# Kernel optimization log

Hardware: AMD Instinct MI355X
Metric: run time of the kernel (lower is better)

The kernel has to match this reference:

```python
import jax, jax.numpy as jnp
import numpy as np

N_NODES = 50000
N_EDGES = 1600000
IN_DIM = 512
HID = 128  # conv1 out = 2*HID = 256, conv2 out = HID = 128
EPS = 1e-5


def gcn_conv(x, src, dst, W, b, n_nodes):
    """PyG GCNConv: x' = D^{-1/2} (A + I) D^{-1/2} (x W) + b (self loops added)."""
    h = x @ W  # [N, out]
    loop = jnp.arange(n_nodes, dtype=src.dtype)
    s = jnp.concatenate([src, loop])  # sources incl. self loops
    d = jnp.concatenate([dst, loop])  # targets incl. self loops
    ones = jnp.ones(s.shape[0], dtype=h.dtype)
    deg = jax.ops.segment_sum(ones, d, num_segments=n_nodes)  # in-degree on targets
    dis = jnp.where(deg > 0, jax.lax.rsqrt(jnp.maximum(deg, 1.0)), 0.0)
    norm = dis[s] * dis[d]  # [E+N]
    msg = norm[:, None] * h[s]  # gather + scale, [E+N, out]
    out = jax.ops.segment_sum(msg, d, num_segments=n_nodes)  # scatter-add
    return out + b


def batch_norm(x, gamma, beta):
    """BatchNorm1d with batch statistics (biased variance), eps=1e-5."""
    mean = jnp.mean(x, axis=0)
    var = jnp.mean(jnp.square(x - mean), axis=0)
    return (x - mean) * jax.lax.rsqrt(var + EPS) * gamma + beta


def setup_inputs() -> dict:
    key = jax.random.key(0)
    ks = jax.random.split(key, 8)
    x = jax.random.normal(ks[0], (N_NODES, IN_DIM), dtype=jnp.float32)
    edge_index = jax.random.randint(ks[1], (2, N_EDGES), 0, N_NODES, dtype=jnp.int64)
    d1 = 2 * HID
    W1 = jax.random.normal(ks[2], (IN_DIM, d1), dtype=jnp.float32) / np.sqrt(IN_DIM)
    b1 = jnp.zeros((d1,), dtype=jnp.float32)
    gamma1 = jnp.ones((d1,), dtype=jnp.float32)
    beta1 = jnp.zeros((d1,), dtype=jnp.float32)
    W2 = jax.random.normal(ks[3], (d1, HID), dtype=jnp.float32) / np.sqrt(d1)
    b2 = jnp.zeros((HID,), dtype=jnp.float32)
    gamma2 = jnp.ones((HID,), dtype=jnp.float32)
    beta2 = jnp.zeros((HID,), dtype=jnp.float32)
    return {"x": x, "edge_index": edge_index, "W1": W1, "b1": b1,
            "gamma1": gamma1, "beta1": beta1, "W2": W2, "b2": b2,
            "gamma2": gamma2, "beta2": beta2}


def reference(x, edge_index, W1, b1, gamma1, beta1, W2, b2, gamma2, beta2):
    src, dst = edge_index[0], edge_index[1]
    h = gcn_conv(x, src, dst, W1, b1, N_NODES)
    h = batch_norm(h, gamma1, beta1)
    h = jax.nn.relu(h)
    # dropout: identity in eval mode (deterministic reference)
    h = gcn_conv(h, src, dst, W2, b2, N_NODES)
    h = batch_norm(h, gamma2, beta2)
    return h
```

## Files before the change

kernel.cpp:

```cpp
#include <hip/hip_runtime.h>
#include <hip/hip_bf16.h>


#define NN 50000
#define NE 1600000
#define DIN 512
#define D1 256
#define D2 128
#define EPSV 1e-5f
#define NBUCK 16
#define BSZ 3125
#define NDB 128
#define NPB 391
#define CAP 16384

typedef __attribute__((ext_vector_type(8))) short bf16x8_t;
typedef __attribute__((ext_vector_type(4))) float f32x4_t;

__device__ __forceinline__ float bf2f(unsigned short u) {
  return __uint_as_float(((unsigned int)u) << 16);
}
__device__ __forceinline__ unsigned short f2bf(float f) {
  unsigned int u = __float_as_uint(f);
  u += 0x7fffu + ((u >> 16) & 1u);
  return (unsigned short)(u >> 16);
}
__device__ __forceinline__ unsigned int pk2(float a, float b) {
  __hip_bfloat162 h = __float22bfloat162_rn(make_float2(a, b));
  union { __hip_bfloat162 h; unsigned int u; } c;
  c.h = h;
  return c.u;
}

__global__ __launch_bounds__(256) void k_part_prep(const int* __restrict__ src,
                                                   const int* __restrict__ dst,
                                                   int* __restrict__ gcursor,
                                                   unsigned int* __restrict__ part,
                                                   const float* __restrict__ W1,
                                                   const float* __restrict__ W2,
                                                   unsigned short* __restrict__ W1t,
                                                   unsigned short* __restrict__ W2t) {
  __shared__ int hist[NDB];
  __shared__ int curs[NDB];
  const int t = threadIdx.x;
  if (blockIdx.x < 256) {
    const int EB = NE / 256;
    const int e0 = blockIdx.x * EB;
    if (t < NDB) hist[t] = 0;
    __syncthreads();
    for (int i = t; i < EB; i += 256) {
      int d = dst[e0 + i];
      atomicAdd(&hist[d / NPB], 1);
    }
    __syncthreads();
    if (t < NDB) {
      int c = hist[t];
      curs[t] = (c > 0) ? atomicAdd(&gcursor[t], c) : 0;
    }
    __syncthreads();
    for (int i = t; i < EB; i += 256) {
      int s = src[e0 + i];
      int d = dst[e0 + i];
      int b = d / NPB;
      int dl = d - b * NPB;
      int sb = (unsigned)s / BSZ;
      unsigned int w = (unsigned)s | ((unsigned)dl << 16) | ((unsigned)sb << 25);
      int pos = atomicAdd(&curs[b], 1);
      if (pos < CAP) part[(size_t)b * CAP + pos] = w;
    }
  } else {
    int i = (blockIdx.x - 256) * 256 + t;
    if (i < DIN * D1) {
      int n = i / DIN, k = i - n * DIN;
      W1t[i] = f2bf(W1[(size_t)k * D1 + n]);
    } else {
      int j = i - DIN * D1;
      int n = j / D1, k = j - n * D1;
      W2t[j] = f2bf(W2[(size_t)k * D2 + n]);
    }
  }
}

__global__ void k_bscan(const int* __restrict__ gcursor, int* __restrict__ ebase) {
  __shared__ int s[NDB];
  int t = threadIdx.x;
  int v = gcursor[t];
  s[t] = v;
  __syncthreads();
  for (int off = 1; off < NDB; off <<= 1) {
    int a = (t >= off) ? s[t - off] : 0;
    __syncthreads();
    s[t] += a;
    __syncthreads();
  }
  ebase[t] = s[t] - v;
  if (t == NDB - 1) ebase[NDB] = s[t];
}

__global__ __launch_bounds__(256) void k_build_gemm1(const unsigned int* __restrict__ part,
                                                     const int* __restrict__ gcursor,
                                                     const int* __restrict__ ebase,
                                                     int* __restrict__ row_ptr,
                                                     float* __restrict__ dis,
                                                     int* __restrict__ col,
                                                     const float* __restrict__ A,
                                                     const unsigned short* __restrict__ Bt,
                                                     unsigned short* __restrict__ C, int M) {
  __shared__ __align__(16) char smem[40960];
  const int t = threadIdx.x;
  if (blockIdx.x < NDB) {
    const int NC = NPB * NBUCK;
    int* cnt = (int*)smem;
    int* tsum = (int*)(smem + 25024);
    const int b = blockIdx.x;
    int m = gcursor[b];
    if (m > CAP) m = CAP;
    const int base = ebase[b];
    const unsigned int* my = part + (size_t)b * CAP;
    for (int i = t; i < NC; i += 256) cnt[i] = 0;
    __syncthreads();
    for (int i = t; i < m; i += 256) {
      unsigned int w = my[i];
      atomicAdd(&cnt[((w >> 16) & 0x1ff) * NBUCK + (w >> 25)], 1);
    }
    __syncthreads();
    const int CHK = (NC + 255) / 256;
    int i0 = t * CHK;
    int sum = 0;
    for (int i = 0; i < CHK; i++) {
      int idx = i0 + i;
      if (idx < NC) sum += cnt[idx];
    }
    tsum[t] = sum;
    __syncthreads();
    for (int off = 1; off < 256; off <<= 1) {
      int a = (t >= off) ? tsum[t - off] : 0;
      __syncthreads();
      tsum[t] += a;
      __syncthreads();
    }
    int run = tsum[t] - sum;
    for (int i = 0; i < CHK; i++) {
      int idx = i0 + i;
      if (idx < NC) {
        int c = cnt[idx];
        cnt[idx] = run;
        run += c;
      }
    }
    __syncthreads();
    const int n0 = b * NPB;
    for (int dl = t; dl < NPB; dl += 256) {
      int n = n0 + dl;
      if (n < NN) {
        int st = cnt[dl * NBUCK];
        int en = (dl * NBUCK + NBUCK < NC) ? cnt[dl * NBUCK + NBUCK] : m;
        row_ptr[n] = base + st;
        dis[n] = rsqrtf((float)(en - st + 1));
      }
    }
    if (b == NDB - 1 && t == 0) row_ptr[NN] = base + m;
    __syncthreads();
    for (int i = t; i < m; i += 256) {
      unsigned int w = my[i];
      int pos = atomicAdd(&cnt[((w >> 16) & 0x1ff) * NBUCK + (w >> 25)], 1);
      col[base + pos] = w & 0xffff;
    }
  } else {
    unsigned short* As = (unsigned short*)smem;
    unsigned short* Bs = (unsigned short*)(smem + 8192);
    const int wave = t >> 6, lane = t & 63;
    const int m0 = (blockIdx.x - NDB) * 64;
    const int wn = wave * 64;
    const int l8 = lane >> 3;
    const int lbs = (lane & 7) ^ l8;
    const int row_c = lane & 15, quad = lane >> 4;

    f32x4_t acc[4][4];
#pragma unroll
    for (int i = 0; i < 4; i++)
#pragma unroll
      for (int j = 0; j < 4; j++) acc[i][j] = (f32x4_t){0.f, 0.f, 0.f, 0.f};

    for (int k0 = 0; k0 < DIN; k0 += 64) {
#pragma unroll
      for (int j = 0; j < 8; j++) {
        int chunk = wave * 8 + j;
        int row = chunk * 8 + l8;
        const unsigned short* g = Bt + (size_t)row * DIN + k0 + lbs * 8;
        __builtin_amdgcn_global_load_lds(
            (const __attribute__((address_space(1))) unsigned int*)g,
            (__attribute__((address_space(3))) unsigned int*)(Bs + chunk * 512), 16, 0, 0);
      }
#pragma unroll
      for (int i = 0; i < 2; i++) {
        int bid = i * 256 + t;
        int row = bid >> 3, pb = bid & 7;
        int lb = pb ^ (row & 7);
        int gm = m0 + row;
        if (gm >= M) gm = M - 1;
        const float4* s = (const float4*)(A + (size_t)gm * DIN + k0 + lb * 8);
        float4 v0 = s[0], v1 = s[1];
        uint4 o;
        o.x = pk2(v0.x, v0.y);
        o.y = pk2(v0.z, v0.w);
        o.z = pk2(v1.x, v1.y);
        o.w = pk2(v1.z, v1.w);
        *(uint4*)(As + row * 64 + pb * 8) = o;
      }
      __syncthreads();
#pragma unroll
      for (int ki = 0; ki < 2; ki++) {
        bf16x8_t af[4], bfr[4];
        int kb = ki * 4 + quad;
#pragma unroll
        for (int i = 0; i < 4; i++) {
          int ar = i * 16 + row_c;
          af[i] = *(const bf16x8_t*)(As + ar * 64 + ((kb ^ (ar & 7)) * 8));
          int br = wn + i * 16 + row_c;
          bfr[i] = *(const bf16x8_t*)(Bs + br * 64 + ((kb ^ (br & 7)) * 8));
        }
#pragma unroll
        for (int i = 0; i < 4; i++)
#pragma unroll
          for (int j = 0; j < 4; j++)
            acc[i][j] = __builtin_amdgcn_mfma_f32_16x16x32_bf16(af[i], bfr[j], acc[i][j], 0, 0, 0);
      }
      __syncthreads();
    }
#pragma unroll
    for (int i = 0; i < 4; i++) {
#pragma unroll
      for (int j = 0; j < 4; j++) {
        int colv = wn + j * 16 + row_c;
#pragma unroll
        for (int r = 0; r < 4; r++) {
          int gm = m0 + i * 16 + quad * 4 + r;
          if (gm < M) C[(size_t)gm * D1 + colv] = f2bf(acc[i][j][r]);
        }
      }
    }
  }
}

__global__ void k_finalize1(const float* __restrict__ stats, const float* __restrict__ gamma,
                            const float* __restrict__ beta, float* __restrict__ sc1,
                            float* __restrict__ sh1) {
  int c = threadIdx.x;
  float mean = stats[c] * (1.0f / NN);
  float var = stats[D1 + c] * (1.0f / NN) - mean * mean;
  float sc = gamma[c] * rsqrtf(var + EPSV);
  sc1[c] = sc;
  sh1[c] = beta[c] - mean * sc;
}

__global__ __launch_bounds__(128) void k_gemm2(const unsigned short* __restrict__ A,
                                               const float* __restrict__ sc1,
                                               const float* __restrict__ sh1,
                                               const unsigned short* __restrict__ Bt,
                                               unsigned short* __restrict__ C, int M) {
  __shared__ unsigned short As[64 * 64];
  __shared__ unsigned short Bs[128 * 64];
  const int t = threadIdx.x;
  const int wave = t >> 6, lane = t & 63;
  const int m0 = blockIdx.x * 64;
  const int wn = wave * 64;
  const int l8 = lane >> 3;
  const int lbs = (lane & 7) ^ l8;
  const int row_c = lane & 15, quad = lane >> 4;

  f32x4_t acc[4][4];
#pragma unroll
  for (int i = 0; i < 4; i++)
#pragma unroll
    for (int j = 0; j < 4; j++) acc[i][j] = (f32x4_t){0.f, 0.f, 0.f, 0.f};

  for (int k0 = 0; k0 < D1; k0 += 64) {
#pragma unroll
    for (int j = 0; j < 8; j++) {
      int chunk = wave * 8 + j;
      int row = chunk * 8 + l8;
      const unsigned short* g = Bt + (size_t)row * D1 + k0 + lbs * 8;
      __builtin_amdgcn_global_load_lds(
          (const __attribute__((address_space(1))) unsigned int*)g,
          (__attribute__((address_space(3))) unsigned int*)(Bs + chunk * 512), 16, 0, 0);
    }
#pragma unroll
    for (int i = 0; i < 4; i++) {
      int bid = i * 128 + t;
      int row = bid >> 3, pb = bid & 7;
      int lb = pb ^ (row & 7);
      int gm = m0 + row;
      if (gm >= M) gm = M - 1;
      int colb = k0 + lb * 8;
      uint4 raw = *(const uint4*)(A + (size_t)gm * D1 + colb);
      float4 scA = *(const float4*)(sc1 + colb);
      float4 scB = *(const float4*)(sc1 + colb + 4);
      float4 shA = *(const float4*)(sh1 + colb);
      float4 shB = *(const float4*)(sh1 + colb + 4);
      float f0 = fmaxf(fmaf(bf2f((unsigned short)(raw.x & 0xffff)), scA.x, shA.x), 0.f);
      float f1 = fmaxf(fmaf(bf2f((unsigned short)(raw.x >> 16)),    scA.y, shA.y), 0.f);
      float f2 = fmaxf(fmaf(bf2f((unsigned short)(raw.y & 0xffff)), scA.z, shA.z), 0.f);
      float f3 = fmaxf(fmaf(bf2f((unsigned short)(raw.y >> 16)),    scA.w, shA.w), 0.f);
      float f4 = fmaxf(fmaf(bf2f((unsigned short)(raw.z & 0xffff)), scB.x, shB.x), 0.f);
      float f5 = fmaxf(fmaf(bf2f((unsigned short)(raw.z >> 16)),    scB.y, shB.y), 0.f);
      float f6 = fmaxf(fmaf(bf2f((unsigned short)(raw.w & 0xffff)), scB.z, shB.z), 0.f);
      float f7 = fmaxf(fmaf(bf2f((unsigned short)(raw.w >> 16)),    scB.w, shB.w), 0.f);
      uint4 o;
      o.x = pk2(f0, f1);
      o.y = pk2(f2, f3);
      o.z = pk2(f4, f5);
      o.w = pk2(f6, f7);
      *(uint4*)(As + row * 64 + pb * 8) = o;
    }
    __syncthreads();
#pragma unroll
    for (int ki = 0; ki < 2; ki++) {
      bf16x8_t af[4], bfr[4];
      int kb = ki * 4 + quad;
#pragma unroll
      for (int i = 0; i < 4; i++) {
        int ar = i * 16 + row_c;
        af[i] = *(const bf16x8_t*)(As + ar * 64 + ((kb ^ (ar & 7)) * 8));
        int br = wn + i * 16 + row_c;
        bfr[i] = *(const bf16x8_t*)(Bs + br * 64 + ((kb ^ (br & 7)) * 8));
      }
#pragma unroll
      for (int i = 0; i < 4; i++)
#pragma unroll
        for (int j = 0; j < 4; j++)
          acc[i][j] = __builtin_amdgcn_mfma_f32_16x16x32_bf16(af[i], bfr[j], acc[i][j], 0, 0, 0);
    }
    __syncthreads();
  }
#pragma unroll
  for (int i = 0; i < 4; i++) {
#pragma unroll
    for (int j = 0; j < 4; j++) {
      int colv = wn + j * 16 + row_c;
#pragma unroll
      for (int r = 0; r < 4; r++) {
        int gm = m0 + i * 16 + quad * 4 + r;
        if (gm < M) C[(size_t)gm * D2 + colv] = f2bf(acc[i][j][r]);
      }
    }
  }
}

__global__ __launch_bounds__(256) void k_agg1h(const unsigned short* __restrict__ H,
                                               const int* __restrict__ row_ptr,
                                               const int* __restrict__ col,
                                               const float* __restrict__ dis,
                                               const float* __restrict__ bias,
                                               unsigned short* __restrict__ OUT,
                                               int half) {
  int n = blockIdx.x * 4 + (threadIdx.x >> 6);
  int lane = threadIdx.x & 63;
  if (n >= NN) return;
  const unsigned short* Hh = H + half * 128;
  float dn = dis[n];
  ushort2 v = ((const ushort2*)(Hh + (size_t)n * D1))[lane];
  float wsf = dn * dn;
  float a0 = wsf * bf2f(v.x), a1 = wsf * bf2f(v.y);
  int e = row_ptr[n], e1 = row_ptr[n + 1];
  while (e < e1) {
    int cnt = e1 - e;
    if (cnt > 64) cnt = 64;
    int li = (lane < cnt) ? lane : (cnt - 1);
    int cv = col[e + li];
    float dwv = dis[cv] * dn;
    int dwu = __float_as_int(dwv);
    int b = 0;
    for (; b + 8 <= cnt; b += 8) {
      int s[8];
      float w[8];
      ushort2 u[8];
#pragma unroll
      for (int k = 0; k < 8; k++) {
        s[k] = __builtin_amdgcn_readlane(cv, b + k);
        w[k] = __int_as_float(__builtin_amdgcn_readlane(dwu, b + k));
      }
#pragma unroll
      for (int k = 0; k < 8; k++)
        u[k] = ((const ushort2*)(Hh + (size_t)s[k] * D1))[lane];
#pragma unroll
      for (int k = 0; k < 8; k++) {
        a0 += w[k] * bf2f(u[k].x);
        a1 += w[k] * bf2f(u[k].y);
      }
    }
    for (; b < cnt; b++) {
      int sK = __builtin_amdgcn_readlane(cv, b);
      float wK = __int_as_float(__builtin_amdgcn_readlane(dwu, b));
      ushort2 uK = ((const ushort2*)(Hh + (size_t)sK * D1))[lane];
      a0 += wK * bf2f(uK.x);
      a1 += wK * bf2f(uK.y);
    }
    e += cnt;
  }
  int c = half * 128 + lane * 2;
  a0 += bias[c]; a1 += bias[c + 1];
  ushort2 o;
  o.x = f2bf(a0); o.y = f2bf(a1);
  ((ushort2*)(OUT + (size_t)n * D1 + half * 128))[lane] = o;
}

__global__ __launch_bounds__(256) void k_agg2(const unsigned short* __restrict__ H,
                                              const int* __restrict__ row_ptr,
                                              const int* __restrict__ col,
                                              const float* __restrict__ dis,
                                              const float* __restrict__ bias,
                                              float* __restrict__ OUT) {
  int n = blockIdx.x * 4 + (threadIdx.x >> 6);
  int lane = threadIdx.x & 63;
  if (n >= NN) return;
  float dn = dis[n];
  ushort2 v = ((const ushort2*)(H + (size_t)n * D2))[lane];
  float wsf = dn * dn;
  float a0 = wsf * bf2f(v.x), a1 = wsf * bf2f(v.y);
  int e = row_ptr[n], e1 = row_ptr[n + 1];
  while (e < e1) {
    int cnt = e1 - e;
    if (cnt > 64) cnt = 64;
    int li = (lane < cnt) ? lane : (cnt - 1);
    int cv = col[e + li];
    float dwv = dis[cv] * dn;
    int dwu = __float_as_int(dwv);
    int b = 0;
    for (; b + 8 <= cnt; b += 8) {
      int s[8];
      float w[8];
      ushort2 u[8];
#pragma unroll
      for (int k = 0; k < 8; k++) {
        s[k] = __builtin_amdgcn_readlane(cv, b + k);
        w[k] = __int_as_float(__builtin_amdgcn_readlane(dwu, b + k));
      }
#pragma unroll
      for (int k = 0; k < 8; k++)
        u[k] = ((const ushort2*)(H + (size_t)s[k] * D2))[lane];
#pragma unroll
      for (int k = 0; k < 8; k++) {
        a0 += w[k] * bf2f(u[k].x);
        a1 += w[k] * bf2f(u[k].y);
      }
    }
    for (; b < cnt; b++) {
      int sK = __builtin_amdgcn_readlane(cv, b);
      float wK = __int_as_float(__builtin_amdgcn_readlane(dwu, b));
      ushort2 uK = ((const ushort2*)(H + (size_t)sK * D2))[lane];
      a0 += wK * bf2f(uK.x);
      a1 += wK * bf2f(uK.y);
    }
    e += cnt;
  }
  int c = lane * 2;
  a0 += bias[c]; a1 += bias[c + 1];
  ((float2*)(OUT + (size_t)n * D2))[lane] = make_float2(a0, a1);
}

__global__ void k_stats1(const unsigned short* __restrict__ X, float* __restrict__ stats) {
  int t = threadIdx.x;
  int r0 = blockIdx.x * 64;
  int r1 = (r0 + 64 < NN) ? r0 + 64 : NN;
  float s = 0.f, q = 0.f;
  for (int r = r0; r < r1; r++) {
    float v = bf2f(X[(size_t)r * D1 + t]);
    s += v;
    q += v * v;
  }
  atomicAdd(&stats[t], s);
  atomicAdd(&stats[D1 + t], q);
}

__global__ void k_stats2(const float* __restrict__ X, float* __restrict__ stats) {
  int t = threadIdx.x;
  int r0 = blockIdx.x * 128;
  int r1 = (r0 + 128 < NN) ? r0 + 128 : NN;
  float s = 0.f, q = 0.f;
  for (int r = r0; r < r1; r++) {
    float v = X[(size_t)r * D2 + t];
    s += v;
    q += v * v;
  }
  atomicAdd(&stats[t], s);
  atomicAdd(&stats[D2 + t], q);
}

__global__ void k_apply2(float* __restrict__ X, const float* __restrict__ stats,
                         const float* __restrict__ gamma, const float* __restrict__ beta) {
  int i = blockIdx.x * blockDim.x + threadIdx.x;
  int c = i & (D2 - 1);
  float mean = stats[c] * (1.0f / NN);
  float var = stats[D2 + c] * (1.0f / NN) - mean * mean;
  float sc = gamma[c] * rsqrtf(var + EPSV);
  X[i] = (X[i] - mean) * sc + beta[c];
}

extern "C" void kernel_launch(void* const* d_in, const int* in_sizes, int n_in,
                              void* d_out, int out_size, void* d_ws, size_t ws_size,
                              hipStream_t stream) {
  const float* x  = (const float*)d_in[0];
  const int* ei   = (const int*)d_in[1];
  const int* srcv = ei;
  const int* dstv = ei + NE;
  const float* W1  = (const float*)d_in[2];
  const float* b1  = (const float*)d_in[3];
  const float* g1  = (const float*)d_in[4];
  const float* be1 = (const float*)d_in[5];
  const float* W2  = (const float*)d_in[6];
  const float* b2  = (const float*)d_in[7];
  const float* g2  = (const float*)d_in[8];
  const float* be2 = (const float*)d_in[9];
  float* out = (float*)d_out;

  char* ws = (char*)d_ws;
  size_t off = 0;
  auto alloc = [&](size_t bytes) {
    size_t cur = off;
    off = (off + bytes + 255) & ~(size_t)255;
    return cur;
  };
  int* gcursor   = (int*)(ws + alloc(NDB * 4));
  float* stats   = (float*)(ws + alloc((D1 * 2 + D2 * 2) * 4));
  int* row_ptr   = (int*)(ws + alloc((NN + 1) * 4));
  float* dis     = (float*)(ws + alloc(NN * 4));
  int* ebase     = (int*)(ws + alloc((NDB + 1) * 4));
  float* sc1     = (float*)(ws + alloc(D1 * 4));
  float* sh1     = (float*)(ws + alloc(D1 * 4));
  int* col       = (int*)(ws + alloc((size_t)NE * 4));
  unsigned int* part = (unsigned int*)(ws + alloc((size_t)NDB * CAP * 4));
  unsigned short* H1  = (unsigned short*)(ws + alloc((size_t)NN * D1 * 2));
  unsigned short* A1  = (unsigned short*)(ws + alloc((size_t)NN * D1 * 2));
  unsigned short* H2  = (unsigned short*)(ws + alloc((size_t)NN * D2 * 2));
  unsigned short* W1t = (unsigned short*)(ws + alloc((size_t)DIN * D1 * 2));
  unsigned short* W2t = (unsigned short*)(ws + alloc((size_t)D1 * D2 * 2));
  float* stats2 = stats + D1 * 2;

  hipMemsetAsync(gcursor, 0, NDB * 4 + (D1 * 2 + D2 * 2) * 4, stream);

  k_part_prep<<<256 + 640, 256, 0, stream>>>(srcv, dstv, gcursor, part, W1, W2, W1t, W2t);
  k_bscan<<<1, NDB, 0, stream>>>(gcursor, ebase);

  const int mb = (NN + 63) / 64;

  k_build_gemm1<<<NDB + mb, 256, 0, stream>>>(part, gcursor, ebase, row_ptr, dis, col,
                                              x, W1t, H1, NN);

  k_agg1h<<<(NN + 3) / 4, 256, 0, stream>>>(H1, row_ptr, col, dis, b1, A1, 0);
  k_agg1h<<<(NN + 3) / 4, 256, 0, stream>>>(H1, row_ptr, col, dis, b1, A1, 1);
  k_stats1<<<(NN + 63) / 64, 256, 0, stream>>>(A1, stats);
  k_finalize1<<<1, 256, 0, stream>>>(stats, g1, be1, sc1, sh1);

  k_gemm2<<<mb, 128, 0, stream>>>(A1, sc1, sh1, W2t, H2, NN);
  k_agg2<<<(NN + 3) / 4, 256, 0, stream>>>(H2, row_ptr, col, dis, b2, out);
  k_stats2<<<(NN + 127) / 128, 128, 0, stream>>>(out, stats2);
  k_apply2<<<NN * D2 / 256, 256, 0, stream>>>(out, stats2, g2, be2);
}
```

Measured before the change: 494.1 us.

## Double destination partitions and fold BN1 finalize into gemm2 prologue

Increases the number of destination partitions from 128 to 256 (fewer nodes per partition, smaller per-partition capacity), so the CSR build phase spreads over more blocks with smaller shared-memory histograms. Separately, removes the single-block finalize kernel and recomputes the batch-norm scale and shift inline in gemm2 from the raw statistics, gamma and beta. This saves one launch and a serial dependency, at the cost of redundant rsqrt work per loaded A tile and a lower per-partition capacity. That capacity drops to 10240 against an expected ~6250 edges per partition, so overflow is unlikely but still possible.

```diff
diff --git a/kernel.cpp b/kernel.cpp
--- a/kernel.cpp
+++ b/kernel.cpp
@@ -10,9 +10,9 @@
 #define EPSV 1e-5f
 #define NBUCK 16
 #define BSZ 3125
-#define NDB 128
-#define NPB 391
-#define CAP 16384
+#define NDB 256
+#define NPB 196
+#define CAP 10240
 
 typedef __attribute__((ext_vector_type(8))) short bf16x8_t;
 typedef __attribute__((ext_vector_type(4))) float f32x4_t;
@@ -46,14 +46,14 @@
   if (blockIdx.x < 256) {
     const int EB = NE / 256;
     const int e0 = blockIdx.x * EB;
-    if (t < NDB) hist[t] = 0;
+    hist[t] = 0;
     __syncthreads();
     for (int i = t; i < EB; i += 256) {
       int d = dst[e0 + i];
       atomicAdd(&hist[d / NPB], 1);
     }
     __syncthreads();
-    if (t < NDB) {
+    {
       int c = hist[t];
       curs[t] = (c > 0) ? atomicAdd(&gcursor[t], c) : 0;
     }
@@ -111,7 +111,7 @@
   if (blockIdx.x < NDB) {
     const int NC = NPB * NBUCK;
     int* cnt = (int*)smem;
-    int* tsum = (int*)(smem + 25024);
+    int* tsum = (int*)(smem + 12544);
     const int b = blockIdx.x;
     int m = gcursor[b];
     if (m > CAP) m = CAP;
@@ -243,20 +243,10 @@
   }
 }
 
-__global__ void k_finalize1(const float* __restrict__ stats, const float* __restrict__ gamma,
-                            const float* __restrict__ beta, float* __restrict__ sc1,
-                            float* __restrict__ sh1) {
-  int c = threadIdx.x;
-  float mean = stats[c] * (1.0f / NN);
-  float var = stats[D1 + c] * (1.0f / NN) - mean * mean;
-  float sc = gamma[c] * rsqrtf(var + EPSV);
-  sc1[c] = sc;
-  sh1[c] = beta[c] - mean * sc;
-}
-
 __global__ __launch_bounds__(128) void k_gemm2(const unsigned short* __restrict__ A,
-                                               const float* __restrict__ sc1,
-                                               const float* __restrict__ sh1,
+                                               const float* __restrict__ stats,
+                                               const float* __restrict__ gamma,
+                                               const float* __restrict__ beta,
                                                const unsigned short* __restrict__ Bt,
                                                unsigned short* __restrict__ C, int M) {
   __shared__ unsigned short As[64 * 64];
@@ -294,18 +284,37 @@
       if (gm >= M) gm = M - 1;
       int colb = k0 + lb * 8;
       uint4 raw = *(const uint4*)(A + (size_t)gm * D1 + colb);
-      float4 scA = *(const float4*)(sc1 + colb);
-      float4 scB = *(const float4*)(sc1 + colb + 4);
-      float4 shA = *(const float4*)(sh1 + colb);
-      float4 shB = *(const float4*)(sh1 + colb + 4);
-      float f0 = fmaxf(fmaf(bf2f((unsigned short)(raw.x & 0xffff)), scA.x, shA.x), 0.f);
-      float f1 = fmaxf(fmaf(bf2f((unsigned short)(raw.x >> 16)),    scA.y, shA.y), 0.f);
-      float f2 = fmaxf(fmaf(bf2f((unsigned short)(raw.y & 0xffff)), scA.z, shA.z), 0.f);
-      float f3 = fmaxf(fmaf(bf2f((unsigned short)(raw.y >> 16)),    scA.w, shA.w), 0.f);
-      float f4 = fmaxf(fmaf(bf2f((unsigned short)(raw.z & 0xffff)), scB.x, shB.x), 0.f);
-      float f5 = fmaxf(fmaf(bf2f((unsigned short)(raw.z >> 16)),    scB.y, shB.y), 0.f);
-      float f6 = fmaxf(fmaf(bf2f((unsigned short)(raw.w & 0xffff)), scB.z, shB.z), 0.f);
-      float f7 = fmaxf(fmaf(bf2f((unsigned short)(raw.w >> 16)),    scB.w, shB.w), 0.f);
+      float4 s0 = *(const float4*)(stats + colb);
+      float4 s1 = *(const float4*)(stats + colb + 4);
+      float4 q0 = *(const float4*)(stats + D1 + colb);
+      float4 q1 = *(const float4*)(stats + D1 + colb + 4);
+      float4 gA = *(const float4*)(gamma + colb);
+      float4 gB = *(const float4*)(gamma + colb + 4);
+      float4 bA = *(const float4*)(beta + colb);
+      float4 bB = *(const float4*)(beta + colb + 4);
+      const float inv = 1.0f / NN;
+      float m0v = s0.x * inv, m1 = s0.y * inv, m2 = s0.z * inv, m3 = s0.w * inv;
+      float m4 = s1.x * inv, m5 = s1.y * inv, m6 = s1.z * inv, m7 = s1.w * inv;
+      float c0 = gA.x * rsqrtf(q0.x * inv - m0v * m0v + EPSV);
+      float c1 = gA.y * rsqrtf(q0.y * inv - m1 * m1 + EPSV);
+      float c2 = gA.z * rsqrtf(q0.z * inv - m2 * m2 + EPSV);
+      float c3 = gA.w * rsqrtf(q0.w * inv - m3 * m3 + EPSV);
+      float c4 = gB.x * rsqrtf(q1.x * inv - m4 * m4 + EPSV);
+      float c5 = gB.y * rsqrtf(q1.y * inv - m5 * m5 + EPSV);
+      float c6 = gB.z * rsqrtf(q1.z * inv - m6 * m6 + EPSV);
+      float c7 = gB.w * rsqrtf(q1.w * inv - m7 * m7 + EPSV);
+      float h0 = bA.x - m0v * c0, h1 = bA.y - m1 * c1;
+      float h2 = bA.z - m2 * c2, h3 = bA.w - m3 * c3;
+      float h4 = bB.x - m4 * c4, h5 = bB.y - m5 * c5;
+      float h6 = bB.z - m6 * c6, h7 = bB.w - m7 * c7;
+      float f0 = fmaxf(fmaf(bf2f((unsigned short)(raw.x & 0xffff)), c0, h0), 0.f);
+      float f1 = fmaxf(fmaf(bf2f((unsigned short)(raw.x >> 16)),    c1, h1), 0.f);
+      float f2 = fmaxf(fmaf(bf2f((unsigned short)(raw.y & 0xffff)), c2, h2), 0.f);
+      float f3 = fmaxf(fmaf(bf2f((unsigned short)(raw.y >> 16)),    c3, h3), 0.f);
+      float f4 = fmaxf(fmaf(bf2f((unsigned short)(raw.z & 0xffff)), c4, h4), 0.f);
+      float f5 = fmaxf(fmaf(bf2f((unsigned short)(raw.z >> 16)),    c5, h5), 0.f);
+      float f6 = fmaxf(fmaf(bf2f((unsigned short)(raw.w & 0xffff)), c6, h6), 0.f);
+      float f7 = fmaxf(fmaf(bf2f((unsigned short)(raw.w >> 16)),    c7, h7), 0.f);
       uint4 o;
       o.x = pk2(f0, f1);
       o.y = pk2(f2, f3);
@@ -526,8 +535,6 @@
   int* row_ptr   = (int*)(ws + alloc((NN + 1) * 4));
   float* dis     = (float*)(ws + alloc(NN * 4));
   int* ebase     = (int*)(ws + alloc((NDB + 1) * 4));
-  float* sc1     = (float*)(ws + alloc(D1 * 4));
-  float* sh1     = (float*)(ws + alloc(D1 * 4));
   int* col       = (int*)(ws + alloc((size_t)NE * 4));
   unsigned int* part = (unsigned int*)(ws + alloc((size_t)NDB * CAP * 4));
   unsigned short* H1  = (unsigned short*)(ws + alloc((size_t)NN * D1 * 2));
@@ -550,9 +557,8 @@
   k_agg1h<<<(NN + 3) / 4, 256, 0, stream>>>(H1, row_ptr, col, dis, b1, A1, 0);
   k_agg1h<<<(NN + 3) / 4, 256, 0, stream>>>(H1, row_ptr, col, dis, b1, A1, 1);
   k_stats1<<<(NN + 63) / 64, 256, 0, stream>>>(A1, stats);
-  k_finalize1<<<1, 256, 0, stream>>>(stats, g1, be1, sc1, sh1);
-
-  k_gemm2<<<mb, 128, 0, stream>>>(A1, sc1, sh1, W2t, H2, NN);
+
+  k_gemm2<<<mb, 128, 0, stream>>>(A1, stats, g1, be1, W2t, H2, NN);
   k_agg2<<<(NN + 3) / 4, 256, 0, stream>>>(H2, row_ptr, col, dis, b2, out);
   k_stats2<<<(NN + 127) / 128, 128, 0, stream>>>(out, stats2);
   k_apply2<<<NN * D2 / 256, 256, 0, stream>>>(out, stats2, g2, be2);
```

After: 496.1 us. Within noise of the previous version (+0.4%).

## Double destination buckets, fold bucket scan into build kernel, merge agg1 halves

Applied to the files above, without the earlier changes.

Raises the number of destination partitions from 128 to 256, with fewer nodes and a smaller capacity per partition, so the CSR build spreads across more blocks and uses less shared memory. The separate single-block prefix-scan kernel is removed, and each build block redundantly scans the global bucket counts itself. The two half-width layer-1 aggregation launches become one launch with twice the grid. Together these cut kernel launches and serialization gaps, at the cost of the redundant per-block scan and a tighter per-bucket capacity that could overflow on skewed inputs.

```diff
diff --git a/kernel.cpp b/kernel.cpp
--- a/kernel.cpp
+++ b/kernel.cpp
@@ -10,9 +10,10 @@
 #define EPSV 1e-5f
 #define NBUCK 16
 #define BSZ 3125
-#define NDB 128
-#define NPB 391
-#define CAP 16384
+#define NDB 256
+#define NPB 196
+#define CAP 10240
+#define AGB ((NN + 3) / 4)
 
 typedef __attribute__((ext_vector_type(8))) short bf16x8_t;
 typedef __attribute__((ext_vector_type(4))) float f32x4_t;
@@ -46,14 +47,14 @@
   if (blockIdx.x < 256) {
     const int EB = NE / 256;
     const int e0 = blockIdx.x * EB;
-    if (t < NDB) hist[t] = 0;
+    hist[t] = 0;
     __syncthreads();
     for (int i = t; i < EB; i += 256) {
       int d = dst[e0 + i];
       atomicAdd(&hist[d / NPB], 1);
     }
     __syncthreads();
-    if (t < NDB) {
+    {
       int c = hist[t];
       curs[t] = (c > 0) ? atomicAdd(&gcursor[t], c) : 0;
     }
@@ -81,25 +82,8 @@
   }
 }
 
-__global__ void k_bscan(const int* __restrict__ gcursor, int* __restrict__ ebase) {
-  __shared__ int s[NDB];
-  int t = threadIdx.x;
-  int v = gcursor[t];
-  s[t] = v;
-  __syncthreads();
-  for (int off = 1; off < NDB; off <<= 1) {
-    int a = (t >= off) ? s[t - off] : 0;
-    __syncthreads();
-    s[t] += a;
-    __syncthreads();
-  }
-  ebase[t] = s[t] - v;
-  if (t == NDB - 1) ebase[NDB] = s[t];
-}
-
 __global__ __launch_bounds__(256) void k_build_gemm1(const unsigned int* __restrict__ part,
                                                      const int* __restrict__ gcursor,
-                                                     const int* __restrict__ ebase,
                                                      int* __restrict__ row_ptr,
                                                      float* __restrict__ dis,
                                                      int* __restrict__ col,
@@ -109,13 +93,24 @@
   __shared__ __align__(16) char smem[40960];
   const int t = threadIdx.x;
   if (blockIdx.x < NDB) {
+    int* gsc = (int*)smem;
+    const int b = blockIdx.x;
+    int vb = gcursor[b];
+    gsc[t] = gcursor[t];
+    __syncthreads();
+    for (int off = 1; off < NDB; off <<= 1) {
+      int a = (t >= off) ? gsc[t - off] : 0;
+      __syncthreads();
+      gsc[t] += a;
+      __syncthreads();
+    }
+    const int base = gsc[b] - vb;
+    int m = vb;
+    if (m > CAP) m = CAP;
+    __syncthreads();
     const int NC = NPB * NBUCK;
     int* cnt = (int*)smem;
-    int* tsum = (int*)(smem + 25024);
-    const int b = blockIdx.x;
-    int m = gcursor[b];
-    if (m > CAP) m = CAP;
-    const int base = ebase[b];
+    int* tsum = (int*)(smem + 12544);
     const unsigned int* my = part + (size_t)b * CAP;
     for (int i = t; i < NC; i += 256) cnt[i] = 0;
     __syncthreads();
@@ -347,14 +342,15 @@
   }
 }
 
-__global__ __launch_bounds__(256) void k_agg1h(const unsigned short* __restrict__ H,
-                                               const int* __restrict__ row_ptr,
-                                               const int* __restrict__ col,
-                                               const float* __restrict__ dis,
-                                               const float* __restrict__ bias,
-                                               unsigned short* __restrict__ OUT,
-                                               int half) {
-  int n = blockIdx.x * 4 + (threadIdx.x >> 6);
+__global__ __launch_bounds__(256) void k_agg1(const unsigned short* __restrict__ H,
+                                              const int* __restrict__ row_ptr,
+                                              const int* __restrict__ col,
+                                              const float* __restrict__ dis,
+                                              const float* __restrict__ bias,
+                                              unsigned short* __restrict__ OUT) {
+  int bid = blockIdx.x;
+  int half = (bid >= AGB) ? 1 : 0;
+  int n = (bid - half * AGB) * 4 + (threadIdx.x >> 6);
   int lane = threadIdx.x & 63;
   if (n >= NN) return;
   const unsigned short* Hh = H + half * 128;
@@ -525,7 +521,6 @@
   float* stats   = (float*)(ws + alloc((D1 * 2 + D2 * 2) * 4));
   int* row_ptr   = (int*)(ws + alloc((NN + 1) * 4));
   float* dis     = (float*)(ws + alloc(NN * 4));
-  int* ebase     = (int*)(ws + alloc((NDB + 1) * 4));
   float* sc1     = (float*)(ws + alloc(D1 * 4));
   float* sh1     = (float*)(ws + alloc(D1 * 4));
   int* col       = (int*)(ws + alloc((size_t)NE * 4));
@@ -540,15 +535,13 @@
   hipMemsetAsync(gcursor, 0, NDB * 4 + (D1 * 2 + D2 * 2) * 4, stream);
 
   k_part_prep<<<256 + 640, 256, 0, stream>>>(srcv, dstv, gcursor, part, W1, W2, W1t, W2t);
-  k_bscan<<<1, NDB, 0, stream>>>(gcursor, ebase);
 
   const int mb = (NN + 63) / 64;
 
-  k_build_gemm1<<<NDB + mb, 256, 0, stream>>>(part, gcursor, ebase, row_ptr, dis, col,
+  k_build_gemm1<<<NDB + mb, 256, 0, stream>>>(part, gcursor, row_ptr, dis, col,
                                               x, W1t, H1, NN);
 
-  k_agg1h<<<(NN + 3) / 4, 256, 0, stream>>>(H1, row_ptr, col, dis, b1, A1, 0);
-  k_agg1h<<<(NN + 3) / 4, 256, 0, stream>>>(H1, row_ptr, col, dis, b1, A1, 1);
+  k_agg1<<<2 * AGB, 256, 0, stream>>>(H1, row_ptr, col, dis, b1, A1);
   k_stats1<<<(NN + 63) / 64, 256, 0, stream>>>(A1, stats);
   k_finalize1<<<1, 256, 0, stream>>>(stats, g1, be1, sc1, sh1);
 
```

Result: faster. 479.8 us (-2.9%).
